# Performance work log

Measured on AMD Instinct MI355X. Metric: run time of the kernel, lower is better.

The kernel has to match this reference:

```python
import jax, jax.numpy as jnp
import numpy as np

D_MODEL = 2048
EXPAND = 2
D_INNER = EXPAND * D_MODEL          # 4096 == d_ssm
D_STATE = 128
NGROUPS = 1
HEADDIM = 64
NHEADS = D_INNER // HEADDIM          # 64
D_CONV = 4
CHUNK = 128
D_XBC = D_INNER + 2 * NGROUPS * D_STATE   # 4352
D_IN_PROJ = 2 * D_INNER + 2 * NGROUPS * D_STATE + NHEADS  # 8512
EPS = 1e-5


def setup_inputs() -> dict:
    key = jax.random.key(0)
    ks = jax.random.split(key, 9)
    u = jax.random.normal(ks[0], (2, 2048, D_MODEL), dtype=jnp.float32)
    W_in = jax.random.normal(ks[1], (D_IN_PROJ, D_MODEL), dtype=jnp.float32) / np.sqrt(D_MODEL)
    conv_w = jax.random.normal(ks[2], (D_XBC, D_CONV), dtype=jnp.float32) / np.sqrt(D_CONV)
    conv_b = jax.random.normal(ks[3], (D_XBC,), dtype=jnp.float32) * 0.1
    dt_bias = jnp.log(jnp.expm1(jax.random.uniform(ks[4], (NHEADS,), minval=0.001, maxval=0.1)))
    A_log = jnp.log(jax.random.uniform(ks[5], (NHEADS,), minval=1.0, maxval=16.0))
    D = jnp.ones((NHEADS,), dtype=jnp.float32)
    norm_weight = jnp.ones((D_INNER,), dtype=jnp.float32)
    W_out = jax.random.normal(ks[8], (D_MODEL, D_INNER), dtype=jnp.float32) / np.sqrt(D_INNER)
    return {"u": u, "W_in": W_in, "conv_w": conv_w, "conv_b": conv_b,
            "dt_bias": dt_bias, "A_log": A_log, "D": D,
            "norm_weight": norm_weight, "W_out": W_out}


def _causal_conv1d(xBC, conv_w, conv_b):
    # xBC: [b, l, d]; depthwise causal conv of width D_CONV, then SiLU
    x = jnp.transpose(xBC, (0, 2, 1))                      # [b, d, l]
    x = jnp.pad(x, ((0, 0), (0, 0), (D_CONV - 1, 0)))
    y = jax.lax.conv_general_dilated(
        x, conv_w[:, None, :], window_strides=(1,), padding='VALID',
        feature_group_count=D_XBC, dimension_numbers=('NCH', 'OIH', 'NCH'))
    y = y + conv_b[None, :, None]
    return jnp.transpose(jax.nn.silu(y), (0, 2, 1))        # [b, l, d]


def _ssd(x, dt, A, B, C, D):
    # x: [b,l,h,p]; dt: [b,l,h] (post-softplus); A: [h]; B,C: [b,l,g,n]; D: [h]
    b, L, h, p = x.shape
    n = B.shape[-1]
    c = L // CHUNK
    hpg = h // NGROUPS
    Bh = jnp.repeat(B, hpg, axis=2)                        # [b,l,h,n]
    Ch = jnp.repeat(C, hpg, axis=2)
    xr = x.reshape(b, c, CHUNK, h, p)
    dtr = dt.reshape(b, c, CHUNK, h)
    Br = Bh.reshape(b, c, CHUNK, h, n)
    Cr = Ch.reshape(b, c, CHUNK, h, n)
    xdt = xr * dtr[..., None]                              # [b,c,l,h,p]
    dA = jnp.transpose((dt * A[None, None, :]).reshape(b, c, CHUNK, h), (0, 3, 1, 2))  # [b,h,c,l]
    A_cs = jnp.cumsum(dA, axis=-1)                         # [b,h,c,l]
    # intra-chunk decay matrix L[i,j] = exp(sum_{j+1..i} dA), lower-triangular
    diff = A_cs[..., :, None] - A_cs[..., None, :]         # [b,h,c,l,s]
    mask = jnp.tril(jnp.ones((CHUNK, CHUNK), dtype=bool))
    Lmat = jnp.where(mask, jnp.exp(jnp.where(mask, diff, 0.0)), 0.0)
    Y_diag = jnp.einsum('bclhn,bcshn,bhcls,bcshp->bclhp', Cr, Br, Lmat, xdt)
    decay_states = jnp.exp(A_cs[..., -1:] - A_cs)          # [b,h,c,l]
    states = jnp.einsum('bclhn,bhcl,bclhp->bchpn', Br, decay_states, xdt)
    chunk_decay = jnp.exp(A_cs[..., -1])                   # [b,h,c]
    # inter-chunk recurrence over c chunks
    def step(carry, inp):
        s, d = inp                                         # s:[b,h,p,n], d:[b,h]
        return carry * d[..., None, None] + s, carry
    init = jnp.zeros((b, h, p, n), dtype=x.dtype)
    _, prev = jax.lax.scan(step, init,
                           (jnp.transpose(states, (1, 0, 2, 3, 4)),
                            jnp.transpose(chunk_decay, (2, 0, 1))))
    prev_states = jnp.transpose(prev, (1, 0, 2, 3, 4))     # [b,c,h,p,n]
    Y_off = jnp.einsum('bclhn,bchpn,bhcl->bclhp', Cr, prev_states, jnp.exp(A_cs))
    Y = (Y_diag + Y_off).reshape(b, L, h, p) + x * D[None, None, :, None]
    return Y


def reference(u, W_in, conv_w, conv_b, dt_bias, A_log, D, norm_weight, W_out):
    b, L, _ = u.shape
    zxbcdt = jnp.einsum('bld,ed->ble', u, W_in)            # [b,l,8512]
    z = zxbcdt[..., :D_INNER]
    xBC = zxbcdt[..., D_INNER:D_INNER + D_XBC]
    dt = zxbcdt[..., D_INNER + D_XBC:]                     # [b,l,h]
    xBC = _causal_conv1d(xBC, conv_w, conv_b)
    x = xBC[..., :D_INNER]
    B = xBC[..., D_INNER:D_INNER + NGROUPS * D_STATE].reshape(b, L, NGROUPS, D_STATE)
    C = xBC[..., D_INNER + NGROUPS * D_STATE:].reshape(b, L, NGROUPS, D_STATE)
    dt = jax.nn.softplus(dt + dt_bias[None, None, :])
    A = -jnp.exp(A_log)
    y = _ssd(x.reshape(b, L, NHEADS, HEADDIM), dt, A, B, C, D)
    y = y.reshape(b, L, D_INNER)
    # gated RMSNorm (norm_before_gate=False): norm(y * silu(z))
    yg = y * jax.nn.silu(z)
    y = yg * jax.lax.rsqrt(jnp.mean(yg * yg, axis=-1, keepdims=True) + EPS) * norm_weight
    return jnp.einsum('bld,ed->ble', y, W_out)
```

## Files before the change

### kernel.cpp

```cpp
#include <hip/hip_runtime.h>
#include <cstdint>
#include <cstddef>

#define SEQ     2048
#define NBATCH  2
#define BL      (NBATCH*SEQ)
#define DMODEL  2048
#define DINNER  4096
#define DSTATE  128
#define HEADDIM 64
#define NHEADS  64
#define DXBC    4352
#define DPROJ   8512
#define NPAD    8704
#define NCHUNK  16
#define CHUNKL  128

typedef __bf16 bf16x8_t __attribute__((ext_vector_type(8)));
typedef float f32x4_t __attribute__((ext_vector_type(4)));
typedef unsigned short u16x8_t __attribute__((ext_vector_type(8)));
typedef unsigned short u16x4_t __attribute__((ext_vector_type(4)));
typedef __attribute__((address_space(1))) unsigned int as1_u32;
typedef __attribute__((address_space(3))) unsigned int as3_u32;

__device__ __forceinline__ unsigned short f2bf(float f) {
  unsigned u = __builtin_bit_cast(unsigned, f);
  u += 0x7FFFu + ((u >> 16) & 1u);
  return (unsigned short)(u >> 16);
}
__device__ __forceinline__ float bf2f(unsigned short h) {
  unsigned u = ((unsigned)h) << 16;
  return __builtin_bit_cast(float, u);
}
__device__ __forceinline__ void gload16(const void* g, void* l) {
  __builtin_amdgcn_global_load_lds((const as1_u32*)g, (as3_u32*)l, 16, 0, 0);
}
__device__ __forceinline__ f32x4_t mfma16(u16x8_t a, u16x8_t b, f32x4_t c) {
  return __builtin_amdgcn_mfma_f32_16x16x32_bf16(
      __builtin_bit_cast(bf16x8_t, a), __builtin_bit_cast(bf16x8_t, b), c, 0, 0, 0);
}
__device__ __forceinline__ float siluf(float x) { return x / (1.f + __expf(-x)); }

__global__ __launch_bounds__(256) void cvt_kernel(const float* __restrict__ src,
                                                  unsigned short* __restrict__ dst, int n) {
  int idx = (blockIdx.x * 256 + threadIdx.x) * 4;
  if (idx >= n) return;
  float4 v = *(const float4*)&src[idx];
  u16x4_t o; o[0] = f2bf(v.x); o[1] = f2bf(v.y); o[2] = f2bf(v.z); o[3] = f2bf(v.w);
  *(u16x4_t*)&dst[idx] = o;
}

__global__ __launch_bounds__(256) void cvt_win_kernel(const float* __restrict__ W,
                                                      unsigned short* __restrict__ dst) {
  int idx = (blockIdx.x * 256 + threadIdx.x) * 4;
  if (idx >= NPAD * DMODEL) return;
  int e = idx / DMODEL;
  u16x4_t o;
  if (e < DPROJ) {
    float4 v = *(const float4*)&W[idx];
    o[0] = f2bf(v.x); o[1] = f2bf(v.y); o[2] = f2bf(v.z); o[3] = f2bf(v.w);
  } else {
    o[0] = 0; o[1] = 0; o[2] = 0; o[3] = 0;
  }
  *(u16x4_t*)&dst[idx] = o;
}

template <int WM, bool BF16OUT>
__global__ __launch_bounds__(512, 2) void gemm256_kernel(const unsigned short* __restrict__ A,
                                                         const unsigned short* __restrict__ B,
                                                         void* __restrict__ Cp,
                                                         int M, int N, int K, int gx) {
  constexpr int BM  = 32 * WM;
  constexpr int AUB = BM * 64;
  constexpr int BUB = 16384;
  constexpr int BUF = AUB + BUB;
  constexpr int LA  = AUB / 8192;
  constexpr int LB  = 2;
  constexpr int LT  = LA + LB;
  __shared__ __attribute__((aligned(16))) char lds[4 * BUF];

  const int nwg = gridDim.x;
  const int q8 = nwg >> 3;
  const int lid = blockIdx.x;
  const int newid = (lid & 7) * q8 + (lid >> 3);
  const int band = newid / (gx * 4);
  const int idx  = newid % (gx * 4);
  const int n0 = (idx >> 2) * 256;
  const int m0 = (band * 4 + (idx & 3)) * BM;

  const int t = threadIdx.x, lane = t & 63, w = t >> 6;
  const int wm = w >> 2, wn = w & 3;
  const int NK = K >> 5;
  const int kslot = (lane >> 4) * 16;

  f32x4_t acc[WM][4];
#pragma unroll
  for (int i = 0; i < WM; ++i)
#pragma unroll
    for (int j = 0; j < 4; ++j) acc[i][j] = (f32x4_t){0.f, 0.f, 0.f, 0.f};

  auto stage_unit = [&](int u) {
    if (u >= 2 * NK) return;
    const int Tt = u >> 1;
    char* base = lds + (Tt & 3) * BUF + ((u & 1) ? AUB : 0);
    const unsigned short* G = (u & 1) ? B : A;
    const int g0 = (u & 1) ? n0 : m0;
    const int k0 = Tt << 5;
    if (u & 1) {
#pragma unroll
      for (int i = 0; i < LB; ++i) {
        int o = i * 8192 + t * 16;
        int row = o >> 6;
        int cb = (o & 63) ^ (((row >> 1) & 3) << 4);
        gload16(&G[(size_t)(g0 + row) * K + k0 + (cb >> 1)], base + o);
      }
    } else {
#pragma unroll
      for (int i = 0; i < LA; ++i) {
        int o = i * 8192 + t * 16;
        int row = o >> 6;
        int cb = (o & 63) ^ (((row >> 1) & 3) << 4);
        gload16(&G[(size_t)(g0 + row) * K + k0 + (cb >> 1)], base + o);
      }
    }
  };
  auto rdA = [&](int bq, int mr) -> u16x8_t {
    int row = wm * (BM / 2) + mr * 16 + (lane & 15);
    int byte = bq * BUF + row * 64 + (kslot ^ (((row >> 1) & 3) << 4));
    return *(const u16x8_t*)(lds + byte);
  };
  auto rdB = [&](int bq, int nr) -> u16x8_t {
    int row = wn * 64 + nr * 16 + (lane & 15);
    int byte = bq * BUF + AUB + row * 64 + (kslot ^ (((row >> 1) & 3) << 4));
    return *(const u16x8_t*)(lds + byte);
  };

#pragma unroll
  for (int u = 0; u < 6; ++u) stage_unit(u);

  for (int T = 0; T < NK; ++T) {
    const int bq = T & 3;
    if (T <= NK - 3)      { if constexpr (LT == 4) asm volatile("s_waitcnt vmcnt(8)" ::: "memory");
                            else                   asm volatile("s_waitcnt vmcnt(6)" ::: "memory"); }
    else if (T == NK - 2) { if constexpr (LT == 4) asm volatile("s_waitcnt vmcnt(4)" ::: "memory");
                            else                   asm volatile("s_waitcnt vmcnt(3)" ::: "memory"); }
    else                  asm volatile("s_waitcnt vmcnt(0)" ::: "memory");
    __builtin_amdgcn_s_barrier();
    asm volatile("" ::: "memory");
    __builtin_amdgcn_sched_barrier(0);

    u16x8_t af[WM], bfr[4];
#pragma unroll
    for (int mr = 0; mr < WM; ++mr) af[mr] = rdA(bq, mr);
    bfr[0] = rdB(bq, 0);
    bfr[1] = rdB(bq, 1);
    stage_unit(2 * T + 6);
    __builtin_amdgcn_s_setprio(1);
#pragma unroll
    for (int mr = 0; mr < WM; ++mr) {
      acc[mr][0] = mfma16(af[mr], bfr[0], acc[mr][0]);
      acc[mr][1] = mfma16(af[mr], bfr[1], acc[mr][1]);
    }
    __builtin_amdgcn_s_setprio(0);
    bfr[2] = rdB(bq, 2);
    bfr[3] = rdB(bq, 3);
    stage_unit(2 * T + 7);
    __builtin_amdgcn_s_setprio(1);
#pragma unroll
    for (int mr = 0; mr < WM; ++mr) {
      acc[mr][2] = mfma16(af[mr], bfr[2], acc[mr][2]);
      acc[mr][3] = mfma16(af[mr], bfr[3], acc[mr][3]);
    }
    __builtin_amdgcn_s_setprio(0);
  }

#pragma unroll
  for (int mr = 0; mr < WM; ++mr) {
    const int mbase = m0 + wm * (BM / 2) + mr * 16 + (lane >> 4) * 4;
#pragma unroll
    for (int nr = 0; nr < 4; ++nr) {
      const int n = n0 + wn * 64 + nr * 16 + (lane & 15);
#pragma unroll
      for (int r = 0; r < 4; ++r) {
        if (BF16OUT) ((unsigned short*)Cp)[(size_t)(mbase + r) * N + n] = f2bf(acc[mr][nr][r]);
        else         ((float*)Cp)[(size_t)(mbase + r) * N + n] = acc[mr][nr][r];
      }
    }
  }
}

__global__ __launch_bounds__(256) void conv_kernel(const unsigned short* __restrict__ zx,
                                                   const float* __restrict__ conv_w,
                                                   const float* __restrict__ conv_b,
                                                   unsigned short* __restrict__ xc) {
  int idx = blockIdx.x * 256 + threadIdx.x;
  if (idx >= BL * (DXBC / 8)) return;
  int e8 = (idx % (DXBC / 8)) * 8;
  int bl = idx / (DXBC / 8);
  int l = bl % SEQ, b = bl / SEQ;
  float acc[8];
#pragma unroll
  for (int j = 0; j < 8; ++j) acc[j] = conv_b[e8 + j];
  const unsigned short* zrow = zx + (size_t)b * SEQ * NPAD + DINNER + e8;
#pragma unroll
  for (int wi = 0; wi < 4; ++wi) {
    int ll = l - 3 + wi;
    if (ll >= 0) {
      u16x8_t v = *(const u16x8_t*)(zrow + (size_t)ll * NPAD);
#pragma unroll
      for (int j = 0; j < 8; ++j) acc[j] += bf2f(v[j]) * conv_w[(e8 + j) * 4 + wi];
    }
  }
  u16x8_t o;
#pragma unroll
  for (int j = 0; j < 8; ++j) o[j] = f2bf(siluf(acc[j]));
  *(u16x8_t*)(xc + (size_t)bl * DXBC + e8) = o;
}

__global__ __launch_bounds__(128) void dt_kernel(const unsigned short* __restrict__ zx,
                                                 const float* __restrict__ dt_bias,
                                                 const float* __restrict__ A_log,
                                                 float* __restrict__ dt_soft,
                                                 float* __restrict__ Acs,
                                                 float* __restrict__ cdecay) {
  int blk = blockIdx.x;
  int c = blk & 15, h = (blk >> 4) & 63, b = blk >> 10;
  int i = threadIdx.x;
  int l = c * CHUNKL + i;
  float raw = bf2f(zx[((size_t)b * SEQ + l) * NPAD + (DINNER + DXBC) + h]) + dt_bias[h];
  float dt = (raw > 20.f) ? raw : log1pf(__expf(raw));
  dt_soft[((size_t)b * 64 + h) * SEQ + l] = dt;
  float A = -__expf(A_log[h]);
  __shared__ float sbuf[128];
  sbuf[i] = dt * A;
  __syncthreads();
  for (int ofs = 1; ofs < 128; ofs <<= 1) {
    float v = (i >= ofs) ? sbuf[i - ofs] : 0.f;
    __syncthreads();
    sbuf[i] += v;
    __syncthreads();
  }
  float cs = sbuf[i];
  Acs[(((size_t)b * 64 + h) * 16 + c) * 128 + i] = cs;
  if (i == 127) cdecay[((size_t)b * 64 + h) * 16 + c] = __expf(cs);
}

__global__ __launch_bounds__(256) void xdt_kernel(const unsigned short* __restrict__ xc,
                                                  const float* __restrict__ dt_soft,
                                                  unsigned short* __restrict__ xdtT) {
  int blk = blockIdx.x;
  int lt = blk & 15, h = (blk >> 4) & 63, b = blk >> 10;
  __shared__ unsigned short tile[128][66];
  __shared__ float dts[128];
  int t = threadIdx.x;
  const unsigned short* xg = xc + ((size_t)b * SEQ + lt * 128) * DXBC + h * 64;
#pragma unroll
  for (int k = 0; k < 32; ++k) {
    int idx = t + k * 256;
    int row = idx >> 6, col = idx & 63;
    tile[row][col] = xg[(size_t)row * DXBC + col];
  }
  if (t < 128) dts[t] = dt_soft[((size_t)b * 64 + h) * SEQ + lt * 128 + t];
  __syncthreads();
  unsigned short* xo = xdtT + (((size_t)b * 64 + h) * 64) * SEQ + lt * 128;
#pragma unroll
  for (int k = 0; k < 32; ++k) {
    int idx = t + k * 256;
    int p = idx >> 7, j = idx & 127;
    xo[(size_t)p * SEQ + j] = f2bf(bf2f(tile[j][p]) * dts[j]);
  }
}

__global__ __launch_bounds__(256) void btr_kernel(const unsigned short* __restrict__ xc,
                                                  unsigned short* __restrict__ BT) {
  int blk = blockIdx.x;
  int lt = blk & 15, b = blk >> 4;
  __shared__ unsigned short tile[128][129];
  int t = threadIdx.x;
  const unsigned short* src = xc + ((size_t)b * SEQ + lt * 128) * DXBC + DINNER;
#pragma unroll
  for (int k = 0; k < 64; ++k) {
    int idx = t + k * 256;
    int j = idx >> 7, n = idx & 127;
    tile[j][n] = src[(size_t)j * DXBC + n];
  }
  __syncthreads();
  unsigned short* dst = BT + (size_t)b * 128 * SEQ + lt * 128;
#pragma unroll
  for (int k = 0; k < 64; ++k) {
    int idx = t + k * 256;
    int n = idx >> 7, j = idx & 127;
    dst[(size_t)n * SEQ + j] = tile[j][n];
  }
}

__global__ __launch_bounds__(256) void ssd_states_kernel(const unsigned short* __restrict__ BT,
                                                         const unsigned short* __restrict__ xdtT,
                                                         const float* __restrict__ Acs,
                                                         float* __restrict__ states) {
  int blk = blockIdx.x;
  int h = blk & 63, c = (blk >> 6) & 15, b = blk >> 10;
  __shared__ unsigned short BTs[128 * 128];
  __shared__ unsigned short xs[64 * 128];
  __shared__ float dec[128];
  int t = threadIdx.x, lane = t & 63, w = t >> 6, wr = w >> 1, wc = w & 1;
  int srow = t >> 4, scol = (t & 15) * 8;
  const unsigned short* BTb = BT + (size_t)b * 128 * SEQ + c * 128;
#pragma unroll
  for (int s = 0; s < 8; ++s) {
    int r = s * 16 + srow;
    gload16(&BTb[(size_t)r * SEQ + scol], &BTs[r * 128 + scol]);
  }
  const unsigned short* xb = xdtT + (((size_t)b * 64 + h) * 64) * SEQ + c * 128;
#pragma unroll
  for (int s = 0; s < 4; ++s) {
    int r = s * 16 + srow;
    gload16(&xb[(size_t)r * SEQ + scol], &xs[r * 128 + scol]);
  }
  const float* acsr = Acs + (((size_t)b * 64 + h) * 16 + c) * 128;
  float alast = acsr[127];
  if (t < 128) dec[t] = __expf(alast - acsr[t]);
  __syncthreads();

  f32x4_t acc[2][4];
#pragma unroll
  for (int i = 0; i < 2; ++i)
#pragma unroll
    for (int j = 0; j < 4; ++j) acc[i][j] = (f32x4_t){0.f, 0.f, 0.f, 0.f};
#pragma unroll
  for (int ks = 0; ks < 4; ++ks) {
    const int kk = ks * 32 + (lane >> 4) * 8;
    float d8[8];
#pragma unroll
    for (int e = 0; e < 8; ++e) d8[e] = dec[kk + e];
    u16x8_t af[2], bfr[4];
#pragma unroll
    for (int i = 0; i < 2; ++i) {
      u16x8_t raw = *(const u16x8_t*)&xs[(wr * 32 + i * 16 + (lane & 15)) * 128 + kk];
      u16x8_t sc;
#pragma unroll
      for (int e = 0; e < 8; ++e) sc[e] = f2bf(bf2f(raw[e]) * d8[e]);
      af[i] = sc;
    }
#pragma unroll
    for (int j = 0; j < 4; ++j)
      bfr[j] = *(const u16x8_t*)&BTs[(wc * 64 + j * 16 + (lane & 15)) * 128 + kk];
#pragma unroll
    for (int i = 0; i < 2; ++i)
#pragma unroll
      for (int j = 0; j < 4; ++j) acc[i][j] = mfma16(af[i], bfr[j], acc[i][j]);
  }
  float* so = states + ((((size_t)b * 16 + c) * 64 + h) * 64) * 128;
#pragma unroll
  for (int i = 0; i < 2; ++i) {
    int pbase = wr * 32 + i * 16 + (lane >> 4) * 4;
#pragma unroll
    for (int j = 0; j < 4; ++j) {
      int n = wc * 64 + j * 16 + (lane & 15);
#pragma unroll
      for (int r = 0; r < 4; ++r) so[(size_t)(pbase + r) * 128 + n] = acc[i][j][r];
    }
  }
}

__global__ __launch_bounds__(256) void ssd_scan_kernel(const float* __restrict__ states,
                                                       const float* __restrict__ cdecay,
                                                       unsigned short* __restrict__ prevb) {
  int blk = blockIdx.x;
  int s = blk & 7, h = (blk >> 3) & 63, b = blk >> 9;
  int t = threadIdx.x;
  float carry[4] = {0.f, 0.f, 0.f, 0.f};
  const float* cd = cdecay + ((size_t)b * 64 + h) * 16;
  for (int c = 0; c < 16; ++c) {
    const float* sp = states + (((size_t)(b * 16 + c) * 64 + h) * 64) * 128;
    unsigned short* pp = prevb + (((size_t)(b * 16 + c) * 64 + h) * 64) * 128;
    float d = cd[c];
#pragma unroll
    for (int k = 0; k < 4; ++k) {
      int e = s * 1024 + k * 256 + t;
      pp[e] = f2bf(carry[k]);
      carry[k] = carry[k] * d + sp[e];
    }
  }
}

__global__ __launch_bounds__(256) void ssd_y_kernel(const unsigned short* __restrict__ xc,
                                                    const unsigned short* __restrict__ xdtT,
                                                    const unsigned short* __restrict__ prevb,
                                                    const float* __restrict__ Acs,
                                                    const float* __restrict__ Dp,
                                                    unsigned short* __restrict__ Y) {
  int blk = blockIdx.x;
  int h = blk & 63, c = (blk >> 6) & 15, b = blk >> 10;
  __shared__ unsigned short Bs[128 * 128];
  __shared__ unsigned short Cs[128 * 128];
  __shared__ unsigned short xs[64 * 128];
  __shared__ unsigned short ps[64 * 128];
  __shared__ float acs_s[128];
  int t = threadIdx.x, lane = t & 63, w = t >> 6, wr = w >> 1, wc = w & 1;
  int srow = t >> 4, scol = (t & 15) * 8;
  const unsigned short* Bg = xc + ((size_t)b * SEQ + c * 128) * DXBC + DINNER;
  const unsigned short* Cg = Bg + DSTATE;
#pragma unroll
  for (int s = 0; s < 8; ++s) {
    int r = s * 16 + srow;
    gload16(&Bg[(size_t)r * DXBC + scol], &Bs[r * 128 + scol]);
    gload16(&Cg[(size_t)r * DXBC + scol], &Cs[r * 128 + scol]);
  }
  const unsigned short* xg = xdtT + (((size_t)b * 64 + h) * 64) * SEQ + c * 128;
#pragma unroll
  for (int s = 0; s < 4; ++s) {
    int r = s * 16 + srow;
    gload16(&xg[(size_t)r * SEQ + scol], &xs[r * 128 + scol]);
  }
  const unsigned short* pg = prevb + ((((size_t)b * 16 + c) * 64 + h) * 64) * 128;
#pragma unroll
  for (int s = 0; s < 4; ++s) {
    int r = s * 16 + srow;
    gload16(&pg[r * 128 + scol], &ps[r * 128 + scol]);
  }
  const float* acsr = Acs + (((size_t)b * 64 + h) * 16 + c) * 128;
  if (t < 128) acs_s[t] = acsr[t];
  __syncthreads();

  f32x4_t cbt[4][4];
#pragma unroll
  for (int i = 0; i < 4; ++i)
#pragma unroll
    for (int j = 0; j < 4; ++j) cbt[i][j] = (f32x4_t){0.f, 0.f, 0.f, 0.f};
#pragma unroll
  for (int ks = 0; ks < 4; ++ks) {
    const int kk = ks * 32 + (lane >> 4) * 8;
    u16x8_t af[4], bfr[4];
#pragma unroll
    for (int i = 0; i < 4; ++i) {
      af[i]  = *(const u16x8_t*)&Bs[(wr * 64 + i * 16 + (lane & 15)) * 128 + kk];
      bfr[i] = *(const u16x8_t*)&Cs[(wc * 64 + i * 16 + (lane & 15)) * 128 + kk];
    }
#pragma unroll
    for (int i = 0; i < 4; ++i)
#pragma unroll
      for (int j = 0; j < 4; ++j) cbt[i][j] = mfma16(af[i], bfr[j], cbt[i][j]);
  }
  __syncthreads();
#pragma unroll
  for (int fi = 0; fi < 4; ++fi) {
#pragma unroll
    for (int fj = 0; fj < 4; ++fj) {
      int i = wc * 64 + fj * 16 + (lane & 15);
      int jb = wr * 64 + fi * 16 + (lane >> 4) * 4;
      float ai = acs_s[i];
      u16x4_t m4;
#pragma unroll
      for (int r = 0; r < 4; ++r) {
        int j = jb + r;
        float v = (i >= j) ? cbt[fi][fj][r] * __expf(ai - acs_s[j]) : 0.f;
        m4[r] = f2bf(v);
      }
      *(u16x4_t*)&Bs[i * 128 + jb] = m4;
    }
  }
  __syncthreads();

  f32x4_t accY[4][2], accO[4][2];
#pragma unroll
  for (int i = 0; i < 4; ++i)
#pragma unroll
    for (int j = 0; j < 2; ++j) {
      accY[i][j] = (f32x4_t){0.f, 0.f, 0.f, 0.f};
      accO[i][j] = (f32x4_t){0.f, 0.f, 0.f, 0.f};
    }
#pragma unroll
  for (int ks = 0; ks < 4; ++ks) {
    const int kk = ks * 32 + (lane >> 4) * 8;
    u16x8_t af[4], bfr[2], cf[4], pf[2];
#pragma unroll
    for (int i = 0; i < 4; ++i) {
      af[i] = *(const u16x8_t*)&Bs[(wr * 64 + i * 16 + (lane & 15)) * 128 + kk];
      cf[i] = *(const u16x8_t*)&Cs[(wr * 64 + i * 16 + (lane & 15)) * 128 + kk];
    }
#pragma unroll
    for (int j = 0; j < 2; ++j) {
      bfr[j] = *(const u16x8_t*)&xs[(wc * 32 + j * 16 + (lane & 15)) * 128 + kk];
      pf[j]  = *(const u16x8_t*)&ps[(wc * 32 + j * 16 + (lane & 15)) * 128 + kk];
    }
#pragma unroll
    for (int i = 0; i < 4; ++i)
#pragma unroll
      for (int j = 0; j < 2; ++j) {
        accY[i][j] = mfma16(af[i], bfr[j], accY[i][j]);
        accO[i][j] = mfma16(cf[i], pf[j], accO[i][j]);
      }
  }
  float Dh = Dp[h];
  unsigned short* Yo = Y + ((size_t)b * SEQ + c * 128) * DINNER + h * 64;
  const unsigned short* xo = xc + ((size_t)b * SEQ + c * 128) * DXBC + h * 64;
#pragma unroll
  for (int fi = 0; fi < 4; ++fi) {
    int ibase = wr * 64 + fi * 16 + (lane >> 4) * 4;
#pragma unroll
    for (int r = 0; r < 4; ++r) {
      int i = ibase + r;
      float esc = __expf(acs_s[i]);
#pragma unroll
      for (int fj = 0; fj < 2; ++fj) {
        int p = wc * 32 + fj * 16 + (lane & 15);
        float v = accY[fi][fj][r] + accO[fi][fj][r] * esc + bf2f(xo[(size_t)i * DXBC + p]) * Dh;
        Yo[(size_t)i * DINNER + p] = f2bf(v);
      }
    }
  }
}

__global__ __launch_bounds__(256) void norm_kernel(const unsigned short* __restrict__ Y,
                                                   const unsigned short* __restrict__ zx,
                                                   const float* __restrict__ nw,
                                                   unsigned short* __restrict__ yn) {
  int bl = blockIdx.x;
  const unsigned short* yr = Y + (size_t)bl * DINNER;
  const unsigned short* zr = zx + (size_t)bl * NPAD;
  int t = threadIdx.x;
  float vals[16];
  float ss = 0.f;
#pragma unroll
  for (int k = 0; k < 16; ++k) {
    int d = t + k * 256;
    float g = bf2f(yr[d]) * siluf(bf2f(zr[d]));
    vals[k] = g;
    ss += g * g;
  }
#pragma unroll
  for (int o = 32; o > 0; o >>= 1) ss += __shfl_down(ss, o, 64);
  __shared__ float red[4];
  if ((t & 63) == 0) red[t >> 6] = ss;
  __syncthreads();
  float tot = red[0] + red[1] + red[2] + red[3];
  float rs = rsqrtf(tot * (1.f / (float)DINNER) + 1e-5f);
#pragma unroll
  for (int k = 0; k < 16; ++k) {
    int d = t + k * 256;
    yn[(size_t)bl * DINNER + d] = f2bf(vals[k] * rs * nw[d]);
  }
}

extern "C" void kernel_launch(void* const* d_in, const int* in_sizes, int n_in,
                              void* d_out, int out_size, void* d_ws, size_t ws_size,
                              hipStream_t stream) {
  const float* u       = (const float*)d_in[0];
  const float* W_in    = (const float*)d_in[1];
  const float* conv_w  = (const float*)d_in[2];
  const float* conv_b  = (const float*)d_in[3];
  const float* dt_bias = (const float*)d_in[4];
  const float* A_log   = (const float*)d_in[5];
  const float* Dv      = (const float*)d_in[6];
  const float* norm_w  = (const float*)d_in[7];
  const float* W_out   = (const float*)d_in[8];
  float* out = (float*)d_out;
  (void)in_sizes; (void)n_in; (void)out_size;

  const size_t SZ_UBF    = (size_t)BL * DMODEL * 2;
  const size_t SZ_WIN    = (size_t)NPAD * DMODEL * 2;
  const size_t SZ_XDTT   = (size_t)NBATCH * NHEADS * HEADDIM * SEQ * 2;
  const size_t SZ_ZX     = (size_t)BL * NPAD * 2;
  const size_t SZ_XC     = (size_t)BL * DXBC * 2;
  const size_t SZ_BT     = (size_t)NBATCH * DSTATE * SEQ * 2;
  const size_t SZ_DTS    = (size_t)NBATCH * NHEADS * SEQ * 4;
  const size_t SZ_ACS    = (size_t)NBATCH * NHEADS * NCHUNK * 128 * 4;
  const size_t SZ_CDEC   = (size_t)NBATCH * NHEADS * NCHUNK * 4;
  const size_t SZ_STATES = (size_t)NBATCH * NCHUNK * NHEADS * HEADDIM * DSTATE * 4;
  const size_t SZ_PREV   = (size_t)NBATCH * NCHUNK * NHEADS * HEADDIM * DSTATE * 2;
  const size_t REGION_A  = SZ_UBF + SZ_WIN;

  char* ws = (char*)d_ws;
  size_t off = 0;
  auto alloc = [&](size_t bytes) { char* p = ws + off; off += (bytes + 255) & ~(size_t)255; return p; };

  char* regionA = alloc(REGION_A);
  unsigned short* zx     = (unsigned short*)alloc(SZ_ZX);
  unsigned short* xc     = (unsigned short*)alloc(SZ_XC);
  unsigned short* BT     = (unsigned short*)alloc(SZ_BT);
  float* dt_soft         = (float*)alloc(SZ_DTS);
  float* Acs             = (float*)alloc(SZ_ACS);
  float* cdecay          = (float*)alloc(SZ_CDEC);
  char* statesYb         = alloc(SZ_STATES);
  char* prevYn           = alloc(SZ_PREV);
  if (off > ws_size) return;

  unsigned short* u_bf    = (unsigned short*)regionA;
  unsigned short* win_bf  = (unsigned short*)(regionA + SZ_UBF);
  unsigned short* xdtT    = (unsigned short*)regionA;
  unsigned short* wout_bf = (unsigned short*)(regionA + SZ_XDTT);
  float* states           = (float*)statesYb;
  unsigned short* Yb      = (unsigned short*)statesYb;
  unsigned short* prevb   = (unsigned short*)prevYn;
  unsigned short* yn      = (unsigned short*)prevYn;

  cvt_kernel<<<dim3((BL * DMODEL / 4 + 255) / 256), dim3(256), 0, stream>>>(u, u_bf, BL * DMODEL);
  cvt_win_kernel<<<dim3(NPAD * DMODEL / 4 / 256), dim3(256), 0, stream>>>(W_in, win_bf);

  gemm256_kernel<8, true><<<dim3((NPAD / 256) * (BL / 256)), dim3(512), 0, stream>>>(
      u_bf, win_bf, zx, BL, NPAD, DMODEL, NPAD / 256);

  cvt_kernel<<<dim3((DMODEL * DINNER / 4 + 255) / 256), dim3(256), 0, stream>>>(W_out, wout_bf, DMODEL * DINNER);

  conv_kernel<<<dim3(BL * (DXBC / 8) / 256), dim3(256), 0, stream>>>(zx, conv_w, conv_b, xc);

  dt_kernel<<<dim3(NBATCH * NHEADS * NCHUNK), dim3(128), 0, stream>>>(zx, dt_bias, A_log, dt_soft, Acs, cdecay);

  xdt_kernel<<<dim3(NBATCH * NHEADS * NCHUNK), dim3(256), 0, stream>>>(xc, dt_soft, xdtT);
  btr_kernel<<<dim3(NBATCH * (SEQ / 128)), dim3(256), 0, stream>>>(xc, BT);

  ssd_states_kernel<<<dim3(NBATCH * NCHUNK * NHEADS), dim3(256), 0, stream>>>(BT, xdtT, Acs, states);
  ssd_scan_kernel<<<dim3(NBATCH * NHEADS * 8), dim3(256), 0, stream>>>(states, cdecay, prevb);
  ssd_y_kernel<<<dim3(NBATCH * NCHUNK * NHEADS), dim3(256), 0, stream>>>(xc, xdtT, prevb, Acs, Dv, Yb);

  norm_kernel<<<dim3(BL), dim3(256), 0, stream>>>(Yb, zx, norm_w, yn);

  gemm256_kernel<4, false><<<dim3((DMODEL / 256) * (BL / 128)), dim3(512), 0, stream>>>(
      yn, wout_bf, out, BL, DMODEL, DINNER, DMODEL / 256);
}
```

Before: 597.2 us.

## Store chunk states in bf16, vectorize scan and norm, load prev states into registers

Chunk states are now written as bf16 instead of fp32, which halves the traffic between the states and scan kernels. The scan kernel loads all 16 chunks up front as 4-element vectors. The y kernel loads the previous-state fragments straight from global memory into registers and reads Acs from global instead of staging both in LDS. The gated-RMSNorm kernel moves to 16-element contiguous per-thread vector loads and stores. The trade-off is extra bf16 rounding in the recurrence inputs and uncached global reads of Acs inside the y kernel.

Result: faster. 560.3 us (-6.2%).

```diff
diff --git a/kernel.cpp b/kernel.cpp
--- a/kernel.cpp
+++ b/kernel.cpp
@@ -297,7 +297,7 @@
 __global__ __launch_bounds__(256) void ssd_states_kernel(const unsigned short* __restrict__ BT,
                                                          const unsigned short* __restrict__ xdtT,
                                                          const float* __restrict__ Acs,
-                                                         float* __restrict__ states) {
+                                                         unsigned short* __restrict__ states) {
   int blk = blockIdx.x;
   int h = blk & 63, c = (blk >> 6) & 15, b = blk >> 10;
   __shared__ unsigned short BTs[128 * 128];
@@ -350,7 +350,7 @@
 #pragma unroll
       for (int j = 0; j < 4; ++j) acc[i][j] = mfma16(af[i], bfr[j], acc[i][j]);
   }
-  float* so = states + ((((size_t)b * 16 + c) * 64 + h) * 64) * 128;
+  unsigned short* so = states + ((((size_t)b * 16 + c) * 64 + h) * 64) * 128;
 #pragma unroll
   for (int i = 0; i < 2; ++i) {
     int pbase = wr * 32 + i * 16 + (lane >> 4) * 4;
@@ -358,29 +358,36 @@
     for (int j = 0; j < 4; ++j) {
       int n = wc * 64 + j * 16 + (lane & 15);
 #pragma unroll
-      for (int r = 0; r < 4; ++r) so[(size_t)(pbase + r) * 128 + n] = acc[i][j][r];
-    }
-  }
-}
-
-__global__ __launch_bounds__(256) void ssd_scan_kernel(const float* __restrict__ states,
+      for (int r = 0; r < 4; ++r) so[(size_t)(pbase + r) * 128 + n] = f2bf(acc[i][j][r]);
+    }
+  }
+}
+
+__global__ __launch_bounds__(256) void ssd_scan_kernel(const unsigned short* __restrict__ states,
                                                        const float* __restrict__ cdecay,
                                                        unsigned short* __restrict__ prevb) {
   int blk = blockIdx.x;
   int s = blk & 7, h = (blk >> 3) & 63, b = blk >> 9;
   int t = threadIdx.x;
+  const size_t eoff = (size_t)s * 1024 + t * 4;
+  const float* cd = cdecay + ((size_t)b * 64 + h) * 16;
+  u16x4_t vals[16];
+#pragma unroll
+  for (int c = 0; c < 16; ++c) {
+    const unsigned short* sp = states + (((size_t)(b * 16 + c) * 64 + h) * 64) * 128 + eoff;
+    vals[c] = *(const u16x4_t*)sp;
+  }
   float carry[4] = {0.f, 0.f, 0.f, 0.f};
-  const float* cd = cdecay + ((size_t)b * 64 + h) * 16;
+#pragma unroll
   for (int c = 0; c < 16; ++c) {
-    const float* sp = states + (((size_t)(b * 16 + c) * 64 + h) * 64) * 128;
-    unsigned short* pp = prevb + (((size_t)(b * 16 + c) * 64 + h) * 64) * 128;
+    unsigned short* pp = prevb + (((size_t)(b * 16 + c) * 64 + h) * 64) * 128 + eoff;
+    u16x4_t o;
+#pragma unroll
+    for (int k = 0; k < 4; ++k) o[k] = f2bf(carry[k]);
+    *(u16x4_t*)pp = o;
     float d = cd[c];
 #pragma unroll
-    for (int k = 0; k < 4; ++k) {
-      int e = s * 1024 + k * 256 + t;
-      pp[e] = f2bf(carry[k]);
-      carry[k] = carry[k] * d + sp[e];
-    }
+    for (int k = 0; k < 4; ++k) carry[k] = carry[k] * d + bf2f(vals[c][k]);
   }
 }
 
@@ -395,8 +402,6 @@
   __shared__ unsigned short Bs[128 * 128];
   __shared__ unsigned short Cs[128 * 128];
   __shared__ unsigned short xs[64 * 128];
-  __shared__ unsigned short ps[64 * 128];
-  __shared__ float acs_s[128];
   int t = threadIdx.x, lane = t & 63, w = t >> 6, wr = w >> 1, wc = w & 1;
   int srow = t >> 4, scol = (t & 15) * 8;
   const unsigned short* Bg = xc + ((size_t)b * SEQ + c * 128) * DXBC + DINNER;
@@ -414,13 +419,15 @@
     gload16(&xg[(size_t)r * SEQ + scol], &xs[r * 128 + scol]);
   }
   const unsigned short* pg = prevb + ((((size_t)b * 16 + c) * 64 + h) * 64) * 128;
-#pragma unroll
-  for (int s = 0; s < 4; ++s) {
-    int r = s * 16 + srow;
-    gload16(&pg[r * 128 + scol], &ps[r * 128 + scol]);
+  u16x8_t pf_all[4][2];
+#pragma unroll
+  for (int ks = 0; ks < 4; ++ks) {
+    const int kk = ks * 32 + (lane >> 4) * 8;
+#pragma unroll
+    for (int j = 0; j < 2; ++j)
+      pf_all[ks][j] = *(const u16x8_t*)&pg[(size_t)(wc * 32 + j * 16 + (lane & 15)) * 128 + kk];
   }
   const float* acsr = Acs + (((size_t)b * 64 + h) * 16 + c) * 128;
-  if (t < 128) acs_s[t] = acsr[t];
   __syncthreads();
 
   f32x4_t cbt[4][4];
@@ -449,12 +456,12 @@
     for (int fj = 0; fj < 4; ++fj) {
       int i = wc * 64 + fj * 16 + (lane & 15);
       int jb = wr * 64 + fi * 16 + (lane >> 4) * 4;
-      float ai = acs_s[i];
+      float ai = acsr[i];
       u16x4_t m4;
 #pragma unroll
       for (int r = 0; r < 4; ++r) {
         int j = jb + r;
-        float v = (i >= j) ? cbt[fi][fj][r] * __expf(ai - acs_s[j]) : 0.f;
+        float v = (i >= j) ? cbt[fi][fj][r] * __expf(ai - acsr[j]) : 0.f;
         m4[r] = f2bf(v);
       }
       *(u16x4_t*)&Bs[i * 128 + jb] = m4;
@@ -473,23 +480,21 @@
 #pragma unroll
   for (int ks = 0; ks < 4; ++ks) {
     const int kk = ks * 32 + (lane >> 4) * 8;
-    u16x8_t af[4], bfr[2], cf[4], pf[2];
+    u16x8_t af[4], bfr[2], cf[4];
 #pragma unroll
     for (int i = 0; i < 4; ++i) {
       af[i] = *(const u16x8_t*)&Bs[(wr * 64 + i * 16 + (lane & 15)) * 128 + kk];
       cf[i] = *(const u16x8_t*)&Cs[(wr * 64 + i * 16 + (lane & 15)) * 128 + kk];
     }
 #pragma unroll
-    for (int j = 0; j < 2; ++j) {
+    for (int j = 0; j < 2; ++j)
       bfr[j] = *(const u16x8_t*)&xs[(wc * 32 + j * 16 + (lane & 15)) * 128 + kk];
-      pf[j]  = *(const u16x8_t*)&ps[(wc * 32 + j * 16 + (lane & 15)) * 128 + kk];
-    }
 #pragma unroll
     for (int i = 0; i < 4; ++i)
 #pragma unroll
       for (int j = 0; j < 2; ++j) {
         accY[i][j] = mfma16(af[i], bfr[j], accY[i][j]);
-        accO[i][j] = mfma16(cf[i], pf[j], accO[i][j]);
+        accO[i][j] = mfma16(cf[i], pf_all[ks][j], accO[i][j]);
       }
   }
   float Dh = Dp[h];
@@ -501,7 +506,7 @@
 #pragma unroll
     for (int r = 0; r < 4; ++r) {
       int i = ibase + r;
-      float esc = __expf(acs_s[i]);
+      float esc = __expf(acsr[i]);
 #pragma unroll
       for (int fj = 0; fj < 2; ++fj) {
         int p = wc * 32 + fj * 16 + (lane & 15);
@@ -520,14 +525,20 @@
   const unsigned short* yr = Y + (size_t)bl * DINNER;
   const unsigned short* zr = zx + (size_t)bl * NPAD;
   int t = threadIdx.x;
+  int base = t * 16;
+  u16x8_t y0 = *(const u16x8_t*)&yr[base], y1 = *(const u16x8_t*)&yr[base + 8];
+  u16x8_t z0 = *(const u16x8_t*)&zr[base], z1 = *(const u16x8_t*)&zr[base + 8];
   float vals[16];
   float ss = 0.f;
 #pragma unroll
-  for (int k = 0; k < 16; ++k) {
-    int d = t + k * 256;
-    float g = bf2f(yr[d]) * siluf(bf2f(zr[d]));
-    vals[k] = g;
-    ss += g * g;
+  for (int k = 0; k < 8; ++k) {
+    float g = bf2f(y0[k]) * siluf(bf2f(z0[k]));
+    vals[k] = g; ss += g * g;
+  }
+#pragma unroll
+  for (int k = 0; k < 8; ++k) {
+    float g = bf2f(y1[k]) * siluf(bf2f(z1[k]));
+    vals[8 + k] = g; ss += g * g;
   }
 #pragma unroll
   for (int o = 32; o > 0; o >>= 1) ss += __shfl_down(ss, o, 64);
@@ -536,11 +547,14 @@
   __syncthreads();
   float tot = red[0] + red[1] + red[2] + red[3];
   float rs = rsqrtf(tot * (1.f / (float)DINNER) + 1e-5f);
-#pragma unroll
-  for (int k = 0; k < 16; ++k) {
-    int d = t + k * 256;
-    yn[(size_t)bl * DINNER + d] = f2bf(vals[k] * rs * nw[d]);
-  }
+  u16x8_t o0, o1;
+#pragma unroll
+  for (int k = 0; k < 8; ++k) {
+    o0[k] = f2bf(vals[k] * rs * nw[base + k]);
+    o1[k] = f2bf(vals[8 + k] * rs * nw[base + 8 + k]);
+  }
+  *(u16x8_t*)&yn[(size_t)bl * DINNER + base] = o0;
+  *(u16x8_t*)&yn[(size_t)bl * DINNER + base + 8] = o1;
 }
 
 extern "C" void kernel_launch(void* const* d_in, const int* in_sizes, int n_in,
@@ -567,7 +581,7 @@
   const size_t SZ_DTS    = (size_t)NBATCH * NHEADS * SEQ * 4;
   const size_t SZ_ACS    = (size_t)NBATCH * NHEADS * NCHUNK * 128 * 4;
   const size_t SZ_CDEC   = (size_t)NBATCH * NHEADS * NCHUNK * 4;
-  const size_t SZ_STATES = (size_t)NBATCH * NCHUNK * NHEADS * HEADDIM * DSTATE * 4;
+  const size_t SZ_STATES = (size_t)NBATCH * NCHUNK * NHEADS * HEADDIM * DSTATE * 2;
   const size_t SZ_PREV   = (size_t)NBATCH * NCHUNK * NHEADS * HEADDIM * DSTATE * 2;
   const size_t REGION_A  = SZ_UBF + SZ_WIN;
 
@@ -590,7 +604,7 @@
   unsigned short* win_bf  = (unsigned short*)(regionA + SZ_UBF);
   unsigned short* xdtT    = (unsigned short*)regionA;
   unsigned short* wout_bf = (unsigned short*)(regionA + SZ_XDTT);
-  float* states           = (float*)statesYb;
+  unsigned short* states  = (unsigned short*)statesYb;
   unsigned short* Yb      = (unsigned short*)statesYb;
   unsigned short* prevb   = (unsigned short*)prevYn;
   unsigned short* yn      = (unsigned short*)prevYn;
```
